# Kernel tuning notes

Hardware: AMD Instinct MI355X
Metric: run time of the kernel (lower is better)

The kernel has to match this reference:

```python
import jax, jax.numpy as jnp
import numpy as np


def setup_inputs() -> dict:
    key = jax.random.key(0)
    k1, k2 = jax.random.split(key)
    inp = jax.random.normal(k1, (8, 64, 128, 128), dtype=jnp.float32)
    C = jax.random.normal(k2, (16, 1), dtype=jnp.float32)
    return {"input": inp, "C": C, "sigma": 1}


def reference(input, C, sigma):
    # input: arbitrary shape, C: [L, 1] codebook, sigma: scalar temperature
    x = input.reshape(-1)                      # [N]
    diff = x[None, :] - C                      # [L, N] (C broadcasts [L,1])
    # soft quantize: softmax over L of -sigma * (x - c)^2, weighted sum of codebook
    d_soft = -sigma * diff * diff              # [L, N]
    y = jnp.sum(jax.nn.softmax(d_soft, axis=0) * C, axis=0)  # [N]
    # hard quantize: nearest codebook entry by |x - c|
    idx = jnp.argmin(jnp.abs(diff), axis=0)    # [N]
    hard = C[idx, 0]                           # [N]
    # straight-through: forward = hard, backward flows through soft path y
    out = jax.lax.stop_gradient(hard - y) + y
    return out.reshape(input.shape)
```

## Files before the change

kernel.cpp:

```cpp
#include <hip/hip_runtime.h>
#include <hip/hip_bf16.h>


#define NCODES 16

typedef float vfloat4 __attribute__((ext_vector_type(4)));

__device__ __forceinline__ vfloat4 quant4(vfloat4 v, const float* c) {
    float x0 = v.x, x1 = v.y, x2 = v.z, x3 = v.w;
    float b0 = fabsf(x0 - c[0]), b1 = fabsf(x1 - c[0]);
    float b2 = fabsf(x2 - c[0]), b3 = fabsf(x3 - c[0]);
    float q0 = c[0], q1 = c[0], q2 = c[0], q3 = c[0];
#pragma unroll
    for (int l = 1; l < NCODES; ++l) {
        float cl = c[l];
        float d0 = fabsf(x0 - cl);
        float d1 = fabsf(x1 - cl);
        float d2 = fabsf(x2 - cl);
        float d3 = fabsf(x3 - cl);
        if (d0 < b0) { b0 = d0; q0 = cl; }
        if (d1 < b1) { b1 = d1; q1 = cl; }
        if (d2 < b2) { b2 = d2; q2 = cl; }
        if (d3 < b3) { b3 = d3; q3 = cl; }
    }
    vfloat4 r;
    r.x = q0; r.y = q1; r.z = q2; r.w = q3;
    return r;
}

__global__ __launch_bounds__(256) void stq_main(const vfloat4* __restrict__ in,
                                                vfloat4* __restrict__ out,
                                                const float* __restrict__ C,
                                                int n4,
                                                const float* __restrict__ in_tail,
                                                float* __restrict__ out_tail,
                                                int n_tail) {
    float c[NCODES];
#pragma unroll
    for (int l = 0; l < NCODES; ++l) c[l] = C[l];

    const int stride = gridDim.x * blockDim.x;
    int i = blockIdx.x * blockDim.x + threadIdx.x;

    for (; i + 3 * stride < n4; i += 4 * stride) {
        vfloat4 v0 = in[i];
        vfloat4 v1 = in[i + stride];
        vfloat4 v2 = in[i + 2 * stride];
        vfloat4 v3 = in[i + 3 * stride];
        vfloat4 r0 = quant4(v0, c);
        vfloat4 r1 = quant4(v1, c);
        vfloat4 r2 = quant4(v2, c);
        vfloat4 r3 = quant4(v3, c);
        __builtin_nontemporal_store(r0, &out[i]);
        __builtin_nontemporal_store(r1, &out[i + stride]);
        __builtin_nontemporal_store(r2, &out[i + 2 * stride]);
        __builtin_nontemporal_store(r3, &out[i + 3 * stride]);
    }
    for (; i < n4; i += stride) {
        vfloat4 r = quant4(in[i], c);
        __builtin_nontemporal_store(r, &out[i]);
    }

    int t = blockIdx.x * blockDim.x + threadIdx.x;
    if (t < n_tail) {
        float x = in_tail[t];
        float b = fabsf(x - c[0]);
        float q = c[0];
#pragma unroll
        for (int l = 1; l < NCODES; ++l) {
            float d = fabsf(x - c[l]);
            if (d < b) { b = d; q = c[l]; }
        }
        out_tail[t] = q;
    }
}

extern "C" void kernel_launch(void* const* d_in, const int* in_sizes, int n_in,
                              void* d_out, int out_size, void* d_ws, size_t ws_size,
                              hipStream_t stream) {
    const float* inp = (const float*)d_in[0];
    const float* C   = (const float*)d_in[1];
    float* out = (float*)d_out;

    const int n = in_sizes[0];
    const int n4 = n / 4;
    const int n_tail = n - n4 * 4;

    int blocks = (n4 + 255) / 256;
    if (blocks > 2048) blocks = 2048;
    if (blocks < 1) blocks = 1;

    stq_main<<<blocks, 256, 0, stream>>>((const vfloat4*)inp, (vfloat4*)out, C, n4,
                                         inp + n4 * 4, out + n4 * 4, n_tail);
}
```

Before: 18.68 us.

## Replace nearest-code search with sorted-threshold counting via prep kernel

Adds a one-block prep kernel that sorts the codebook and computes exact float decision thresholds between neighbouring codes by binary search over float ordering, preserving argmin tie-breaking. The main kernel then finds each element's code by counting threshold crossings (15 compares) and looks up the value in shared memory, replacing 15 subtract/abs/compare/select steps per element. The extra kernel launch and its serial work are small, and shared-memory lookups add LDS traffic in exchange for fewer ALU ops in what may be a memory-bound kernel.

```diff
diff --git a/kernel.cpp b/kernel.cpp
--- a/kernel.cpp
+++ b/kernel.cpp
@@ -6,38 +6,78 @@
 
 typedef float vfloat4 __attribute__((ext_vector_type(4)));
 
-__device__ __forceinline__ vfloat4 quant4(vfloat4 v, const float* c) {
-    float x0 = v.x, x1 = v.y, x2 = v.z, x3 = v.w;
-    float b0 = fabsf(x0 - c[0]), b1 = fabsf(x1 - c[0]);
-    float b2 = fabsf(x2 - c[0]), b3 = fabsf(x3 - c[0]);
-    float q0 = c[0], q1 = c[0], q2 = c[0], q3 = c[0];
+__device__ __forceinline__ unsigned f2o(float f) {
+    unsigned u = __float_as_uint(f);
+    return (u & 0x80000000u) ? ~u : (u | 0x80000000u);
+}
+__device__ __forceinline__ float o2f(unsigned o) {
+    unsigned u = (o & 0x80000000u) ? (o & 0x7fffffffu) : ~o;
+    return __uint_as_float(u);
+}
+
+__global__ void stq_prep(const float* __restrict__ C, float* __restrict__ ws, int L) {
+    __shared__ float s_val[NCODES];
+    __shared__ int   s_idx[NCODES];
+    int t = threadIdx.x;
+
+    if (t == 0) {
+        float v[NCODES]; int id[NCODES];
+        for (int i = 0; i < L; ++i) { v[i] = C[i]; id[i] = i; }
+        for (int i = 1; i < L; ++i) {
+            float x = v[i]; int xi = id[i]; int j = i - 1;
+            while (j >= 0 && v[j] > x) { v[j+1] = v[j]; id[j+1] = id[j]; --j; }
+            v[j+1] = x; id[j+1] = xi;
+        }
+        for (int i = 0; i < L; ++i) { s_val[i] = v[i]; s_idx[i] = id[i]; }
+    }
+    __syncthreads();
+
+    if (t < L) ws[t] = s_val[t];
+
+    if (t < L - 1) {
+        float a = s_val[t], b = s_val[t+1];
+        int   ia = s_idx[t], ib = s_idx[t+1];
+        float T;
+        if (a == b) {
+            T = 3.4e38f;
+        } else {
+            unsigned lo = f2o(a), hi = f2o(b);
+            while (hi - lo > 1u) {
+                unsigned mid = lo + (hi - lo) / 2u;
+                float x  = o2f(mid);
+                float da = fabsf(x - a);
+                float db = fabsf(x - b);
+                bool p = (db < da) || (db == da && ib < ia);
+                if (p) hi = mid; else lo = mid;
+            }
+            T = o2f(hi);
+        }
+        ws[NCODES + t] = T;
+    }
+}
+
+__device__ __forceinline__ int idx1(float x, const float* T) {
+    int idx = 0;
 #pragma unroll
-    for (int l = 1; l < NCODES; ++l) {
-        float cl = c[l];
-        float d0 = fabsf(x0 - cl);
-        float d1 = fabsf(x1 - cl);
-        float d2 = fabsf(x2 - cl);
-        float d3 = fabsf(x3 - cl);
-        if (d0 < b0) { b0 = d0; q0 = cl; }
-        if (d1 < b1) { b1 = d1; q1 = cl; }
-        if (d2 < b2) { b2 = d2; q2 = cl; }
-        if (d3 < b3) { b3 = d3; q3 = cl; }
-    }
-    vfloat4 r;
-    r.x = q0; r.y = q1; r.z = q2; r.w = q3;
-    return r;
+    for (int k = 0; k < NCODES - 1; ++k) idx += (x >= T[k]) ? 1 : 0;
+    return idx;
 }
 
 __global__ __launch_bounds__(256) void stq_main(const vfloat4* __restrict__ in,
                                                 vfloat4* __restrict__ out,
-                                                const float* __restrict__ C,
+                                                const float* __restrict__ ws,
                                                 int n4,
                                                 const float* __restrict__ in_tail,
                                                 float* __restrict__ out_tail,
                                                 int n_tail) {
-    float c[NCODES];
+    __shared__ float s_sorted[NCODES];
+
+    float T[NCODES - 1];
 #pragma unroll
-    for (int l = 0; l < NCODES; ++l) c[l] = C[l];
+    for (int k = 0; k < NCODES - 1; ++k) T[k] = ws[NCODES + k];
+
+    if (threadIdx.x < NCODES) s_sorted[threadIdx.x] = ws[threadIdx.x];
+    __syncthreads();
 
     const int stride = gridDim.x * blockDim.x;
     int i = blockIdx.x * blockDim.x + threadIdx.x;
@@ -47,31 +87,33 @@
         vfloat4 v1 = in[i + stride];
         vfloat4 v2 = in[i + 2 * stride];
         vfloat4 v3 = in[i + 3 * stride];
-        vfloat4 r0 = quant4(v0, c);
-        vfloat4 r1 = quant4(v1, c);
-        vfloat4 r2 = quant4(v2, c);
-        vfloat4 r3 = quant4(v3, c);
+
+        vfloat4 r0, r1, r2, r3;
+        r0.x = s_sorted[idx1(v0.x, T)]; r0.y = s_sorted[idx1(v0.y, T)];
+        r0.z = s_sorted[idx1(v0.z, T)]; r0.w = s_sorted[idx1(v0.w, T)];
+        r1.x = s_sorted[idx1(v1.x, T)]; r1.y = s_sorted[idx1(v1.y, T)];
+        r1.z = s_sorted[idx1(v1.z, T)]; r1.w = s_sorted[idx1(v1.w, T)];
+        r2.x = s_sorted[idx1(v2.x, T)]; r2.y = s_sorted[idx1(v2.y, T)];
+        r2.z = s_sorted[idx1(v2.z, T)]; r2.w = s_sorted[idx1(v2.w, T)];
+        r3.x = s_sorted[idx1(v3.x, T)]; r3.y = s_sorted[idx1(v3.y, T)];
+        r3.z = s_sorted[idx1(v3.z, T)]; r3.w = s_sorted[idx1(v3.w, T)];
+
         __builtin_nontemporal_store(r0, &out[i]);
         __builtin_nontemporal_store(r1, &out[i + stride]);
         __builtin_nontemporal_store(r2, &out[i + 2 * stride]);
         __builtin_nontemporal_store(r3, &out[i + 3 * stride]);
     }
     for (; i < n4; i += stride) {
-        vfloat4 r = quant4(in[i], c);
+        vfloat4 v = in[i];
+        vfloat4 r;
+        r.x = s_sorted[idx1(v.x, T)]; r.y = s_sorted[idx1(v.y, T)];
+        r.z = s_sorted[idx1(v.z, T)]; r.w = s_sorted[idx1(v.w, T)];
         __builtin_nontemporal_store(r, &out[i]);
     }
 
     int t = blockIdx.x * blockDim.x + threadIdx.x;
     if (t < n_tail) {
-        float x = in_tail[t];
-        float b = fabsf(x - c[0]);
-        float q = c[0];
-#pragma unroll
-        for (int l = 1; l < NCODES; ++l) {
-            float d = fabsf(x - c[l]);
-            if (d < b) { b = d; q = c[l]; }
-        }
-        out_tail[t] = q;
+        out_tail[t] = s_sorted[idx1(in_tail[t], T)];
     }
 }
 
@@ -81,8 +123,13 @@
     const float* inp = (const float*)d_in[0];
     const float* C   = (const float*)d_in[1];
     float* out = (float*)d_out;
+    float* ws  = (float*)d_ws;
 
     const int n = in_sizes[0];
+    const int L = in_sizes[1];
+
+    stq_prep<<<1, 64, 0, stream>>>(C, ws, L);
+
     const int n4 = n / 4;
     const int n_tail = n - n4 * 4;
 
@@ -90,6 +137,6 @@
     if (blocks > 2048) blocks = 2048;
     if (blocks < 1) blocks = 1;
 
-    stq_main<<<blocks, 256, 0, stream>>>((const vfloat4*)inp, (vfloat4*)out, C, n4,
+    stq_main<<<blocks, 256, 0, stream>>>((const vfloat4*)inp, (vfloat4*)out, ws, n4,
                                          inp + n4 * 4, out + n4 * 4, n_tail);
 }
```

After: 34.40 us. +84.1%, slower.
